# Kernel optimization log

Measured on AMD Instinct MI355X. Metric: run time of the kernel, lower is better.

Reference implementation:

```python
import jax, jax.numpy as jnp
import numpy as np

N = 50000   # nodes
F = 32      # num_node_features
EMB = 32    # embedding_size
R = 8       # num_relations
L = 5       # num_layers
E = 400000  # edges


def setup_inputs() -> dict:
    key = jax.random.key(0)
    ks = jax.random.split(key, 12)
    s = 0.1  # weight scale ~ 1/sqrt(fan_in) for stability over 5 residual layers
    return {
        "x": jax.random.normal(ks[0], (N, F), jnp.float32),
        "edge_index": jax.random.randint(ks[1], (2, E), 0, N, jnp.int32),
        "edge_type": jax.random.randint(ks[2], (E,), 0, R, jnp.int32),
        "edge_dist": jax.random.uniform(ks[3], (E,), jnp.float32),
        "fc_W": jax.random.normal(ks[4], (F, EMB), jnp.float32) * s,
        "fc_b": jnp.zeros((EMB,), jnp.float32),
        "rgcn_W": jax.random.normal(ks[5], (L, R, EMB, EMB), jnp.float32) * s,
        "rgcn_root": jax.random.normal(ks[6], (L, EMB, EMB), jnp.float32) * s,
        "rgcn_bias": jnp.zeros((L, EMB), jnp.float32),
        "mlp_W1": jax.random.normal(ks[7], (1 + R, EMB), jnp.float32) * s,
        "mlp_b1": jnp.zeros((EMB,), jnp.float32),
        "mlp_W2": jax.random.normal(ks[8], (EMB, EMB * EMB), jnp.float32) * s,
        "mlp_b2": jnp.zeros((EMB * EMB,), jnp.float32),
        "nn_root": jax.random.normal(ks[9], (L, EMB, EMB), jnp.float32) * s,
        "nn_bias": jnp.zeros((L, EMB), jnp.float32),
    }


def _forward(x, edge_index, edge_type, edge_dist, fc_W, fc_b, rgcn_W, rgcn_root,
             rgcn_bias, mlp_W1, mlp_b1, mlp_W2, mlp_b2, nn_root, nn_bias):
    n = x.shape[0]
    src, dst = edge_index[0], edge_index[1]  # source_to_target flow

    # edge_attr_c = [distance, onehot(edge_type)] : [E, 1+R]
    onehot = jax.nn.one_hot(edge_type, R, dtype=x.dtype)
    eattr = jnp.concatenate([edge_dist[:, None], onehot], axis=1)

    # Shared edge_mlp -> per-edge [EMB, EMB] weight (same for every NNConv layer)
    We = (jax.nn.relu(eattr @ mlp_W1 + mlp_b1) @ mlp_W2 + mlp_b2).reshape(-1, EMB, EMB)

    # degree for NNConv mean aggregation
    deg = jax.ops.segment_sum(jnp.ones_like(edge_dist), dst, num_segments=n)
    denom = jnp.maximum(deg, 1.0)[:, None]

    # per-relation in-degree for RGCN per-relation mean
    rel_cnt = []
    for r in range(R):
        c = jax.ops.segment_sum((edge_type == r).astype(x.dtype), dst, num_segments=n)
        rel_cnt.append(jnp.maximum(c, 1.0)[:, None])

    h = jax.nn.relu(x @ fc_W + fc_b)
    for l in range(L):
        # RGCNConv: root transform + per-relation mean of W_r x_j
        out = h @ rgcn_root[l] + rgcn_bias[l]
        for r in range(R):
            mask_r = (edge_type == r).astype(h.dtype)[:, None]
            msg = (h @ rgcn_W[l, r])[src] * mask_r  # [E, EMB]
            out = out + jax.ops.segment_sum(msg, dst, num_segments=n) / rel_cnt[r]
        h_disc = jax.nn.relu(out)

        # NNConv: x_j @ Theta(e) per edge, mean-aggregated, + root + bias
        msg = jnp.einsum('ei,eio->eo', h[src], We)  # [E, EMB]
        agg = jax.ops.segment_sum(msg, dst, num_segments=n) / denom
        h_cont = jax.nn.relu(h @ nn_root[l] + agg + nn_bias[l])

        h = h + h_disc + h_cont
    return h


def reference(x, edge_index, edge_type, edge_dist, fc_W, fc_b, rgcn_W, rgcn_root,
              rgcn_bias, mlp_W1, mlp_b1, mlp_W2, mlp_b2, nn_root, nn_bias):
    return _forward(x, edge_index, edge_type, edge_dist, fc_W, fc_b, rgcn_W,
                    rgcn_root, rgcn_bias, mlp_W1, mlp_b1, mlp_W2, mlp_b2,
                    nn_root, nn_bias)
```

## Files before the change

### kernel.cpp

```cpp
#include <hip/hip_runtime.h>

#define N_NODES 50000
#define N_EDGES 400000
#define EMB 32
#define NREL 8
#define NLAYER 5
#define NPB 16
#define NBLK (N_NODES / NPB)
#define KROWS 43
#define NCHUNK 196
#define E2CAP (N_EDGES + 8 * N_NODES)
#define FCB (N_NODES / 8)
#define FILLB ((9 * N_NODES + 255) / 256)
#define WTBFB 83

typedef __attribute__((ext_vector_type(8))) short short8;
typedef __attribute__((ext_vector_type(4))) float f32x4;
typedef __attribute__((ext_vector_type(4))) unsigned int u32x4v;

__device__ __forceinline__ unsigned short f2bf(float f) {
    unsigned u = __float_as_uint(f);
    unsigned r = u + 0x7FFF + ((u >> 16) & 1);
    return (unsigned short)(r >> 16);
}

__device__ __forceinline__ unsigned cvt_pk(float a, float b) {
    unsigned r;
    asm("v_cvt_pk_bf16_f32 %0, %1, %2" : "=v"(r) : "v"(a), "v"(b));
    return r;
}

__device__ __forceinline__ int pdeg_of(int d) {
    return (d > 0 ? d + 7 : 8) & ~7;
}


__global__ __launch_bounds__(256) void setup0_kernel(
    const float* __restrict__ x, const float* __restrict__ fcW, const float* __restrict__ fcb,
    float* __restrict__ h, unsigned short* __restrict__ hb16,
    int* __restrict__ zero9,
    unsigned* __restrict__ hb16a_pad, unsigned* __restrict__ hb16b_pad,
    const float* __restrict__ W2, const float* __restrict__ b2,
    const float* __restrict__ rgcnW, const float* __restrict__ rgcnRoot,
    const float* __restrict__ nnRoot, unsigned short* __restrict__ WB) {
    __shared__ __align__(16) float xt[8][EMB];
    const int b = blockIdx.x, tid = threadIdx.x;
    if (b < FCB) {
        int nl = tid >> 5, lane = tid & 31;
        int n0 = b * 8;
        xt[tid >> 5][tid & 31] = x[n0 * EMB + tid];
        __syncthreads();
        float acc = fcb[lane];
        #pragma unroll
        for (int i = 0; i < EMB; i++) acc += xt[nl][i] * fcW[i * EMB + lane];
        float v = fmaxf(acc, 0.0f);
        int ol = ((lane & 15) << 1) | (lane >> 4);
        h[(size_t)(n0 + nl) * EMB + ol] = v;
        float pv = __shfl_down(v, 16, 32);
        unsigned pk = cvt_pk(v, pv);
        if (lane < 16)
            *(unsigned*)&hb16[(size_t)(n0 + nl) * EMB + 2 * lane] = pk;
    } else if (b < FCB + FILLB) {
        int i = (b - FCB) * 256 + tid;
        if (i < 9 * N_NODES) zero9[i] = 0;
        if (i < EMB / 2) { hb16a_pad[i] = 0u; hb16b_pad[i] = 0u; }
    } else {
        int m = b - FCB - FILLB;
        const float* src;
        if (m < 32) src = W2 + (size_t)m * 1024;
        else if (m == 32) src = b2;
        else {
            int t = m - 33, l = t / 10, j = t % 10;
            src = (j < 8) ? rgcnW + (size_t)(l * 8 + j) * 1024
                : (j == 8) ? rgcnRoot + (size_t)l * 1024
                           : nnRoot + (size_t)l * 1024;
        }
        unsigned short* dst = WB + (size_t)m * 1024;
        #pragma unroll
        for (int c = 0; c < 4; c++) {
            int idx = c * 256 + tid;
            int o = idx >> 5, k = idx & 31;
            int i = (k >> 1) + ((k & 1) << 4);
            dst[o * 32 + k] = f2bf(src[i * 32 + o]);
        }
    }
}

__global__ __launch_bounds__(256) void hist_kernel(const int* __restrict__ ei,
                                                   const int* __restrict__ et,
                                                   int* __restrict__ relcnt) {
    int e = blockIdx.x * 256 + threadIdx.x;
    if (e < N_EDGES) {
        int d = ei[N_EDGES + e];
        atomicAdd(&relcnt[d * NREL + et[e]], 1);
    }
}

__global__ __launch_bounds__(256) void nodeprep_kernel(const int* __restrict__ relcnt,
                                                       int* __restrict__ deg,
                                                       int* __restrict__ bsum,
                                                       float* __restrict__ invdeg,
                                                       float* __restrict__ invcnt,
                                                       unsigned char* __restrict__ perm) {
    __shared__ int wsum[4];
    int tid = threadIdx.x, lane = tid & 63, wv = tid >> 6;
    int i = blockIdx.x * 256 + tid;
    int d = 0;
    if (i < N_NODES) {
        int c0 = relcnt[i * NREL + 0], c1 = relcnt[i * NREL + 1];
        int c2 = relcnt[i * NREL + 2], c3 = relcnt[i * NREL + 3];
        int c4 = relcnt[i * NREL + 4], c5 = relcnt[i * NREL + 5];
        int c6 = relcnt[i * NREL + 6], c7 = relcnt[i * NREL + 7];
        d = c0 + c1 + c2 + c3 + c4 + c5 + c6 + c7;
        deg[i] = d;
        invdeg[i] = 1.0f / (float)(d > 0 ? d : 1);
        invcnt[i * NREL + 0] = 1.0f / (float)(c0 > 0 ? c0 : 1);
        invcnt[i * NREL + 1] = 1.0f / (float)(c1 > 0 ? c1 : 1);
        invcnt[i * NREL + 2] = 1.0f / (float)(c2 > 0 ? c2 : 1);
        invcnt[i * NREL + 3] = 1.0f / (float)(c3 > 0 ? c3 : 1);
        invcnt[i * NREL + 4] = 1.0f / (float)(c4 > 0 ? c4 : 1);
        invcnt[i * NREL + 5] = 1.0f / (float)(c5 > 0 ? c5 : 1);
        invcnt[i * NREL + 6] = 1.0f / (float)(c6 > 0 ? c6 : 1);
        invcnt[i * NREL + 7] = 1.0f / (float)(c7 > 0 ? c7 : 1);
    }
    int v = (i < N_NODES) ? pdeg_of(d) : 0;
    #pragma unroll
    for (int off = 32; off > 0; off >>= 1) v += __shfl_down(v, off, 64);
    if (lane == 0) wsum[wv] = v;
    __syncthreads();
    if (tid == 0) bsum[blockIdx.x] = wsum[0] + wsum[1] + wsum[2] + wsum[3];
    if (i < NBLK) {
        int dd[NPB]; unsigned char idx[NPB];
        #pragma unroll
        for (int k = 0; k < NPB; k++) {
            int s = 0;
            #pragma unroll
            for (int r = 0; r < NREL; r++) s += relcnt[(i * NPB + k) * NREL + r];
            dd[k] = s; idx[k] = (unsigned char)k;
        }
        for (int a = 1; a < NPB; a++) {
            int dv = dd[a]; unsigned char iv = idx[a];
            int j = a - 1;
            while (j >= 0 && dd[j] < dv) { dd[j + 1] = dd[j]; idx[j + 1] = idx[j]; j--; }
            dd[j + 1] = dv; idx[j + 1] = iv;
        }
        #pragma unroll
        for (int k = 0; k < NPB; k++) perm[i * NPB + k] = idx[k];
    }
}

__global__ __launch_bounds__(256) void boff_kernel(const int* __restrict__ bsum,
                                                   int* __restrict__ boff,
                                                   int* __restrict__ row_ptr) {
    __shared__ int ws[4];
    int tid = threadIdx.x, lane = tid & 63, w = tid >> 6;
    int v = (tid < NCHUNK) ? bsum[tid] : 0;
    int incl = v;
    #pragma unroll
    for (int off = 1; off < 64; off <<= 1) {
        int t = __shfl_up(incl, off, 64);
        if (lane >= off) incl += t;
    }
    if (lane == 63) ws[w] = incl;
    __syncthreads();
    int add = 0;
    for (int j = 0; j < w; j++) add += ws[j];
    if (tid < NCHUNK) boff[tid] = add + incl - v;
    if (tid == 0) row_ptr[N_NODES] = ws[0] + ws[1] + ws[2] + ws[3];
}

__global__ __launch_bounds__(256) void rptr_kernel(const int* __restrict__ deg,
                                                   const int* __restrict__ boff,
                                                   int* __restrict__ row_ptr) {
    __shared__ int ws[4];
    int tid = threadIdx.x, lane = tid & 63, w = tid >> 6;
    int i = blockIdx.x * 256 + tid;
    int v = (i < N_NODES) ? pdeg_of(deg[i]) : 0;
    int incl = v;
    #pragma unroll
    for (int off = 1; off < 64; off <<= 1) {
        int t = __shfl_up(incl, off, 64);
        if (lane >= off) incl += t;
    }
    if (lane == 63) ws[w] = incl;
    __syncthreads();
    int add = boff[blockIdx.x];
    for (int j = 0; j < w; j++) add += ws[j];
    if (i < N_NODES) row_ptr[i] = add + incl - v;
}

__global__ __launch_bounds__(256) void scatter_kernel(const int* __restrict__ ei,
                                                      const int* __restrict__ et,
                                                      const float* __restrict__ ed,
                                                      const int* __restrict__ row_ptr,
                                                      const int* __restrict__ deg,
                                                      int* __restrict__ cursor,
                                                      int2* __restrict__ edge2,
                                                      const unsigned char* __restrict__ perm,
                                                      int4* __restrict__ wavetab) {
    int e = blockIdx.x * 256 + threadIdx.x;
    if (e < N_EDGES) {
        int d = ei[N_EDGES + e];
        int pos = row_ptr[d] + atomicAdd(&cursor[d], 1);
        edge2[pos] = make_int2(ei[e] | (et[e] << 16), __float_as_int(ed[e]));
    }
    if (e < N_NODES) {
        int base = row_ptr[e], d = deg[e], pd = pdeg_of(d);
        for (int p = base + d; p < base + pd; ++p)
            edge2[p] = make_int2(N_NODES, 0);
    }
    if (e < NBLK * 8) {
        int b = e >> 3, wv = e & 7;
        int s0 = perm[b * NPB + wv], s1 = perm[b * NPB + (NPB - 1 - wv)];
        int nA = b * NPB + s0, nB = b * NPB + s1;
        int pb0 = row_ptr[nA], pd0 = row_ptr[nA + 1] - pb0;
        int pb1 = row_ptr[nB], pd1 = row_ptr[nB + 1] - pb1;
        wavetab[e] = make_int4(s0 | (s1 << 8), pb0, pb1, pd0 | (pd1 << 16));
    }
}


__device__ __forceinline__ void gath(const unsigned short* __restrict__ hb16, int4 E, int m,
                                     unsigned& uA, unsigned& uB) {
    uA = *(const unsigned*)(hb16 + (((size_t)(E.x & 0xFFFF)) << 5) + 2 * m);
    uB = *(const unsigned*)(hb16 + (((size_t)(E.z & 0xFFFF)) << 5) + 2 * m);
}

__device__ __forceinline__ void proc_pair(int4 E, unsigned uA, unsigned uB,
                                          const float2* wrb2f, float w10_0, float w10_1,
                                          unsigned selm, int m,
                                          unsigned& A0s, unsigned& A1s, unsigned& ASs,
                                          unsigned& B0s, unsigned& B1s) {
    int ra = (E.x >> 16) & 7, rb = (E.z >> 16) & 7;
    float2 wa = wrb2f[ra * 16 + m];
    float2 wb = wrb2f[rb * 16 + m];
    float da = __int_as_float(E.y), db = __int_as_float(E.w);
    float hA0 = fmaxf(fmaf(da, w10_0, wa.x), 0.f);
    float hA1 = fmaxf(fmaf(da, w10_1, wa.y), 0.f);
    float hB0 = fmaxf(fmaf(db, w10_0, wb.x), 0.f);
    float hB1 = fmaxf(fmaf(db, w10_1, wb.y), 0.f);
    A0s = cvt_pk(hA0, hB0);
    A1s = cvt_pk(hA1, hB1);
    ASs = cvt_pk((float)((selm >> ra) & 1u), (float)((selm >> rb) & 1u));
    B0s = (uA & 0xFFFFu) | (uB << 16);
    B1s = (uA >> 16) | (uB & 0xFFFF0000u);
}

__device__ __forceinline__ void mfma6(const unsigned* fa0v, const unsigned* fa1v,
                                      const unsigned* fasv, const unsigned* fb0v,
                                      const unsigned* fb1v,
                                      f32x4& aP00, f32x4& aP01, f32x4& aP10, f32x4& aP11,
                                      f32x4& aS0, f32x4& aS1) {
    u32x4v u0 = {fa0v[0], fa0v[1], fa0v[2], fa0v[3]};
    u32x4v u1 = {fa1v[0], fa1v[1], fa1v[2], fa1v[3]};
    u32x4v us = {fasv[0], fasv[1], fasv[2], fasv[3]};
    u32x4v v0 = {fb0v[0], fb0v[1], fb0v[2], fb0v[3]};
    u32x4v v1 = {fb1v[0], fb1v[1], fb1v[2], fb1v[3]};
    short8 A0 = __builtin_bit_cast(short8, u0);
    short8 A1 = __builtin_bit_cast(short8, u1);
    short8 AS = __builtin_bit_cast(short8, us);
    short8 B0 = __builtin_bit_cast(short8, v0);
    short8 B1 = __builtin_bit_cast(short8, v1);
    aP00 = __builtin_amdgcn_mfma_f32_16x16x32_bf16(A0, B0, aP00, 0, 0, 0);
    aP01 = __builtin_amdgcn_mfma_f32_16x16x32_bf16(A0, B1, aP01, 0, 0, 0);
    aP10 = __builtin_amdgcn_mfma_f32_16x16x32_bf16(A1, B0, aP10, 0, 0, 0);
    aP11 = __builtin_amdgcn_mfma_f32_16x16x32_bf16(A1, B1, aP11, 0, 0, 0);
    aS0  = __builtin_amdgcn_mfma_f32_16x16x32_bf16(AS, B0, aS0, 0, 0, 0);
    aS1  = __builtin_amdgcn_mfma_f32_16x16x32_bf16(AS, B1, aS1, 0, 0, 0);
}

__device__ __forceinline__ void edge_pass(const unsigned short* __restrict__ hb16,
                                          const int2* __restrict__ edge2,
                                          const float2* wrb2f,
                                          int pb, int pe, int quad, int m,
                                          float w10_0, float w10_1, unsigned selm,
                                          int4 E0, unsigned u0A, unsigned u0B,
                                          f32x4& aP00, f32x4& aP01, f32x4& aP10,
                                          f32x4& aP11, f32x4& aS0, f32x4& aS1) {
    {
        unsigned fa0v[4] = {0,0,0,0}, fa1v[4] = {0,0,0,0}, fasv[4] = {0,0,0,0};
        unsigned fb0v[4] = {0,0,0,0}, fb1v[4] = {0,0,0,0};
        proc_pair(E0, u0A, u0B, wrb2f, w10_0, w10_1, selm, m,
                  fa0v[0], fa1v[0], fasv[0], fb0v[0], fb1v[0]);
        if (pb + 8 < pe) {
            int4 E = *(const int4*)&edge2[pb + 8 + quad * 2];
            unsigned uA, uB; gath(hb16, E, m, uA, uB);
            proc_pair(E, uA, uB, wrb2f, w10_0, w10_1, selm, m,
                      fa0v[1], fa1v[1], fasv[1], fb0v[1], fb1v[1]);
        }
        if (pb + 16 < pe) {
            int4 E = *(const int4*)&edge2[pb + 16 + quad * 2];
            unsigned uA, uB; gath(hb16, E, m, uA, uB);
            proc_pair(E, uA, uB, wrb2f, w10_0, w10_1, selm, m,
                      fa0v[2], fa1v[2], fasv[2], fb0v[2], fb1v[2]);
        }
        if (pb + 24 < pe) {
            int4 E = *(const int4*)&edge2[pb + 24 + quad * 2];
            unsigned uA, uB; gath(hb16, E, m, uA, uB);
            proc_pair(E, uA, uB, wrb2f, w10_0, w10_1, selm, m,
                      fa0v[3], fa1v[3], fasv[3], fb0v[3], fb1v[3]);
        }
        mfma6(fa0v, fa1v, fasv, fb0v, fb1v, aP00, aP01, aP10, aP11, aS0, aS1);
    }
    for (int c0 = pb + 32; c0 < pe; c0 += 32) {
        unsigned fa0v[4] = {0,0,0,0}, fa1v[4] = {0,0,0,0}, fasv[4] = {0,0,0,0};
        unsigned fb0v[4] = {0,0,0,0}, fb1v[4] = {0,0,0,0};
        #pragma unroll
        for (int jp = 0; jp < 4; ++jp) {
            if (c0 + jp * 8 < pe) {
                int4 E = *(const int4*)&edge2[c0 + jp * 8 + quad * 2];
                unsigned uA, uB; gath(hb16, E, m, uA, uB);
                proc_pair(E, uA, uB, wrb2f, w10_0, w10_1, selm, m,
                          fa0v[jp], fa1v[jp], fasv[jp], fb0v[jp], fb1v[jp]);
            }
        }
        mfma6(fa0v, fa1v, fasv, fb0v, fb1v, aP00, aP01, aP10, aP11, aS0, aS1);
    }
}

__device__ __forceinline__ void stage_node(unsigned short* __restrict__ P, int quad, int m,
                                           float idg, const float* __restrict__ invcnt_n,
                                           const unsigned short* __restrict__ hb16row,
                                           const f32x4& aP00, const f32x4& aP01,
                                           const f32x4& aP10, const f32x4& aP11,
                                           const f32x4& aS0, const f32x4& aS1) {
    #pragma unroll
    for (int reg = 0; reg < 4; ++reg) {
        const int row = quad * 4 + reg;
        *(unsigned*)&P[row * EMB + 2 * m]        = cvt_pk(aP00[reg] * idg, aP01[reg] * idg);
        *(unsigned*)&P[(row + 16) * EMB + 2 * m] = cvt_pk(aP10[reg] * idg, aP11[reg] * idg);
        if (row <= 8) {
            const float sc = (row == 0) ? idg : invcnt_n[row - 1];
            *(unsigned*)&P[(32 + row) * EMB + 2 * m] = cvt_pk(aS0[reg] * sc, aS1[reg] * sc);
        }
    }
    if (quad < 2) {
        unsigned hh = *(const unsigned*)(hb16row + 2 * m);
        *(unsigned*)&P[(41 + quad) * EMB + 2 * m] = hh;
    }
}

__global__ __launch_bounds__(512, 6) void layer_kernel(
    const float* __restrict__ h,
    const unsigned short* __restrict__ hb16,
    const int2* __restrict__ edge2,
    const int4* __restrict__ wavetab,
    const float* __restrict__ invdeg,
    const float* __restrict__ invcnt,
    const float* __restrict__ W1,
    const float* __restrict__ b1,
    const unsigned short* __restrict__ WBs,
    const unsigned short* __restrict__ WBl,
    const float* __restrict__ rgcnBias_l,
    const float* __restrict__ nnBias_l,
    float* __restrict__ hout,
    unsigned short* __restrict__ hb16out,
    int last)
{
    __shared__ __align__(16) unsigned short P_lds[NPB * KROWS * EMB];
    __shared__ __align__(16) float2 wrb2f[NREL * 16];

    const int tid = threadIdx.x;
    const int n0 = blockIdx.x * NPB;

    if (tid < 128) {
        int r = tid >> 4, mi = tid & 15;
        wrb2f[r * 16 + mi] = make_float2(W1[(1 + r) * EMB + mi] + b1[mi],
                                         W1[(1 + r) * EMB + mi + 16] + b1[mi + 16]);
    }

    const int l    = tid & 63;
    const int w    = tid >> 6;
    const int quad = l >> 4;
    const int m    = l & 15;
    const float w10_0 = W1[m];
    const float w10_1 = W1[m + 16];
    const unsigned selm = (m == 0) ? 0xFFu : (m <= 8 ? (1u << (m - 1)) : 0u);

    int4 wt = wavetab[blockIdx.x * 8 + w];
    const int hw0 = wt.x & 0xFF, hw1 = (wt.x >> 8) & 0xFF;
    const int pb0 = wt.y, pe0 = wt.y + (wt.w & 0xFFFF);
    const int pb1 = wt.z, pe1 = wt.z + (int)((unsigned)wt.w >> 16);
    int4 E0 = *(const int4*)&edge2[pb0 + quad * 2];
    int4 E1 = *(const int4*)&edge2[pb1 + quad * 2];
    unsigned u0A, u0B, u1A, u1B;
    gath(hb16, E0, m, u0A, u0B);
    gath(hb16, E1, m, u1A, u1B);

    __syncthreads();

    {
        f32x4 aP00 = {0,0,0,0}, aP01 = {0,0,0,0}, aP10 = {0,0,0,0}, aP11 = {0,0,0,0};
        f32x4 aS0 = {0,0,0,0}, aS1 = {0,0,0,0};
        edge_pass(hb16, edge2, wrb2f, pb0, pe0, quad, m, w10_0, w10_1, selm,
                  E0, u0A, u0B, aP00, aP01, aP10, aP11, aS0, aS1);
        const int n = n0 + hw0;
        stage_node(P_lds + (size_t)hw0 * KROWS * EMB, quad, m, invdeg[n],
                   invcnt + (size_t)n * NREL, hb16 + (size_t)n * EMB,
                   aP00, aP01, aP10, aP11, aS0, aS1);
    }
    {
        f32x4 aP00 = {0,0,0,0}, aP01 = {0,0,0,0}, aP10 = {0,0,0,0}, aP11 = {0,0,0,0};
        f32x4 aS0 = {0,0,0,0}, aS1 = {0,0,0,0};
        edge_pass(hb16, edge2, wrb2f, pb1, pe1, quad, m, w10_0, w10_1, selm,
                  E1, u1A, u1B, aP00, aP01, aP10, aP11, aS0, aS1);
        const int n = n0 + hw1;
        stage_node(P_lds + (size_t)hw1 * KROWS * EMB, quad, m, invdeg[n],
                   invcnt + (size_t)n * NREL, hb16 + (size_t)n * EMB,
                   aP00, aP01, aP10, aP11, aS0, aS1);
    }
    __syncthreads();

    const int node16 = l & 15;
    const int o0 = l & 15;

    f32x4 accN0 = {0,0,0,0}, accN1 = {0,0,0,0};
    f32x4 accR0 = {0,0,0,0}, accR1 = {0,0,0,0};

    #pragma unroll
    for (int j = 0; j < 6; j++) {
        const int rr = w + 8 * j;
        if (rr < KROWS) {
            const unsigned short* Bsrc = (rr < 33) ? (WBs + (size_t)rr * 1024)
                                                   : (WBl + (size_t)(rr - 33) * 1024);
            short8 bf0 = *(const short8*)(Bsrc + o0 * 32 + quad * 8);
            short8 bf1 = *(const short8*)(Bsrc + (o0 + 16) * 32 + quad * 8);
            short8 a = *(const short8*)&P_lds[(size_t)node16 * KROWS * EMB + rr * EMB + quad * 8];
            if (rr <= 32 || rr == 42) {
                accN0 = __builtin_amdgcn_mfma_f32_16x16x32_bf16(a, bf0, accN0, 0, 0, 0);
                accN1 = __builtin_amdgcn_mfma_f32_16x16x32_bf16(a, bf1, accN1, 0, 0, 0);
            } else {
                accR0 = __builtin_amdgcn_mfma_f32_16x16x32_bf16(a, bf0, accR0, 0, 0, 0);
                accR1 = __builtin_amdgcn_mfma_f32_16x16x32_bf16(a, bf1, accR1, 0, 0, 0);
            }
        }
    }
    __syncthreads();

    float* RedAll = (float*)&P_lds[0];
    {
        float* my = RedAll + w * 1024;
        #pragma unroll
        for (int reg = 0; reg < 4; reg++) {
            int nd = quad * 4 + reg;
            my[nd * 32 + o0]            = accN0[reg];
            my[nd * 32 + o0 + 16]       = accN1[reg];
            my[512 + nd * 32 + o0]      = accR0[reg];
            my[512 + nd * 32 + o0 + 16] = accR1[reg];
        }
    }
    __syncthreads();

    {
        const int hw2 = tid >> 5, lane = tid & 31;
        const int n2 = n0 + hw2;
        float sn = 0.0f, sr = 0.0f;
        #pragma unroll
        for (int ww = 0; ww < 8; ww++) {
            sn += RedAll[ww * 1024 + tid];
            sr += RedAll[ww * 1024 + 512 + tid];
        }
        const int il = ((lane & 15) << 1) | (lane >> 4);
        float hd = h[(size_t)n2 * EMB + il];
        float o_r = fmaxf(sr + rgcnBias_l[lane], 0.0f);
        float o_n = fmaxf(sn + nnBias_l[lane], 0.0f);
        float outv = hd + o_r + o_n;
        hout[(size_t)n2 * EMB + (last ? lane : il)] = outv;
        if (!last) {
            float pv = __shfl_down(outv, 16, 32);
            unsigned pk = cvt_pk(outv, pv);
            if (lane < 16)
                *(unsigned*)&hb16out[(size_t)n2 * EMB + 2 * lane] = pk;
        }
    }
}


extern "C" void kernel_launch(void* const* d_in, const int* in_sizes, int n_in,
                              void* d_out, int out_size, void* d_ws, size_t ws_size,
                              hipStream_t stream) {
    const float* x        = (const float*)d_in[0];
    const int*   ei       = (const int*)d_in[1];
    const int*   et       = (const int*)d_in[2];
    const float* ed       = (const float*)d_in[3];
    const float* fcW      = (const float*)d_in[4];
    const float* fcb      = (const float*)d_in[5];
    const float* rgcnW    = (const float*)d_in[6];
    const float* rgcnRoot = (const float*)d_in[7];
    const float* rgcnBias = (const float*)d_in[8];
    const float* W1       = (const float*)d_in[9];
    const float* b1       = (const float*)d_in[10];
    const float* W2       = (const float*)d_in[11];
    const float* b2       = (const float*)d_in[12];
    const float* nnRoot   = (const float*)d_in[13];
    const float* nnBias   = (const float*)d_in[14];

    float* ws = (float*)d_ws;
    float* h_a    = ws;  ws += (size_t)(N_NODES + 1) * EMB;
    float* h_b    = ws;  ws += (size_t)(N_NODES + 1) * EMB;
    unsigned short* hb16_a = (unsigned short*)ws;  ws += (size_t)(N_NODES + 1) * EMB / 2;
    unsigned short* hb16_b = (unsigned short*)ws;  ws += (size_t)(N_NODES + 1) * EMB / 2;
    float* invdeg = ws;  ws += (size_t)N_NODES;
    float* invcnt = ws;  ws += (size_t)N_NODES * NREL;
    unsigned short* WB = (unsigned short*)ws;  ws += (size_t)83 * 1024 / 2;
    int2* edge2   = (int2*)ws;     ws += (size_t)E2CAP * 2;
    int* row_ptr  = (int*)ws;      ws += (size_t)(N_NODES + 1);
    int* bsum     = (int*)ws;      ws += (size_t)NCHUNK;
    int* boff     = (int*)ws;      ws += (size_t)NCHUNK;
    int* deg      = (int*)ws;      ws += (size_t)N_NODES;
    int* relcnt   = (int*)ws;      ws += (size_t)N_NODES * NREL;
    int* cursor   = (int*)ws;      ws += (size_t)N_NODES;
    unsigned char* perm = (unsigned char*)ws;  ws += (size_t)(NBLK * NPB + 3) / 4;
    int4* wavetab = (int4*)ws;     ws += (size_t)NBLK * 8 * 4;
    (void)in_sizes; (void)n_in; (void)out_size; (void)ws_size;

    setup0_kernel<<<FCB + FILLB + WTBFB, 256, 0, stream>>>(
        x, fcW, fcb, h_a, hb16_a, relcnt,
        (unsigned*)(hb16_a + (size_t)N_NODES * EMB),
        (unsigned*)(hb16_b + (size_t)N_NODES * EMB),
        W2, b2, rgcnW, rgcnRoot, nnRoot, WB);
    hist_kernel<<<(N_EDGES + 255) / 256, 256, 0, stream>>>(ei, et, relcnt);
    nodeprep_kernel<<<NCHUNK, 256, 0, stream>>>(relcnt, deg, bsum, invdeg, invcnt, perm);
    boff_kernel<<<1, 256, 0, stream>>>(bsum, boff, row_ptr);
    rptr_kernel<<<NCHUNK, 256, 0, stream>>>(deg, boff, row_ptr);
    scatter_kernel<<<(N_EDGES + 255) / 256, 256, 0, stream>>>(ei, et, ed, row_ptr, deg,
                                                              cursor, edge2, perm, wavetab);

    const float* hin = h_a;
    const unsigned short* hbin = hb16_a;
    float* houtb = h_b;
    unsigned short* hboutb = hb16_b;
    for (int l = 0; l < NLAYER; l++) {
        int last = (l == NLAYER - 1) ? 1 : 0;
        float* dst = last ? (float*)d_out : houtb;
        layer_kernel<<<NBLK, 512, 0, stream>>>(
            hin, hbin, edge2, wavetab, invdeg, invcnt, W1, b1,
            WB, WB + (size_t)(33 + l * 10) * 1024,
            rgcnBias + (size_t)l * EMB,
            nnBias + (size_t)l * EMB,
            dst, hboutb, last);
        float* old_in = (float*)hin;
        unsigned short* old_hb = (unsigned short*)hbin;
        hin = dst; hbin = hboutb;
        houtb = old_in; hboutb = old_hb;
    }
}
```

Baseline: 368.6 us.

## Use one wave per node with 1024-thread blocks, dropping degree-sorted wave pairing

The layer kernel now launches 16 waves per block, so each wave handles a single node's edges directly through row_ptr. This replaces the earlier scheme of pairing heavy and light nodes per wave from a degree-sorted permutation and wavetab, and the perm and wavetab setup code is removed. The weight-row GEMM loop is split across 16 waves, and the cross-wave reduction gains a second accumulate stage. The LDS table stride is padded from 16 to 17 to avoid bank conflicts. In exchange, load balance within a wave is lost for skewed degrees, and larger blocks may reduce occupancy flexibility.

```diff
diff --git a/kernel.cpp b/kernel.cpp
--- a/kernel.cpp
+++ b/kernel.cpp
@@ -100,8 +100,7 @@
                                                        int* __restrict__ deg,
                                                        int* __restrict__ bsum,
                                                        float* __restrict__ invdeg,
-                                                       float* __restrict__ invcnt,
-                                                       unsigned char* __restrict__ perm) {
+                                                       float* __restrict__ invcnt) {
     __shared__ int wsum[4];
     int tid = threadIdx.x, lane = tid & 63, wv = tid >> 6;
     int i = blockIdx.x * 256 + tid;
@@ -129,24 +128,6 @@
     if (lane == 0) wsum[wv] = v;
     __syncthreads();
     if (tid == 0) bsum[blockIdx.x] = wsum[0] + wsum[1] + wsum[2] + wsum[3];
-    if (i < NBLK) {
-        int dd[NPB]; unsigned char idx[NPB];
-        #pragma unroll
-        for (int k = 0; k < NPB; k++) {
-            int s = 0;
-            #pragma unroll
-            for (int r = 0; r < NREL; r++) s += relcnt[(i * NPB + k) * NREL + r];
-            dd[k] = s; idx[k] = (unsigned char)k;
-        }
-        for (int a = 1; a < NPB; a++) {
-            int dv = dd[a]; unsigned char iv = idx[a];
-            int j = a - 1;
-            while (j >= 0 && dd[j] < dv) { dd[j + 1] = dd[j]; idx[j + 1] = idx[j]; j--; }
-            dd[j + 1] = dv; idx[j + 1] = iv;
-        }
-        #pragma unroll
-        for (int k = 0; k < NPB; k++) perm[i * NPB + k] = idx[k];
-    }
 }
 
 __global__ __launch_bounds__(256) void boff_kernel(const int* __restrict__ bsum,
@@ -195,9 +176,7 @@
                                                       const int* __restrict__ row_ptr,
                                                       const int* __restrict__ deg,
                                                       int* __restrict__ cursor,
-                                                      int2* __restrict__ edge2,
-                                                      const unsigned char* __restrict__ perm,
-                                                      int4* __restrict__ wavetab) {
+                                                      int2* __restrict__ edge2) {
     int e = blockIdx.x * 256 + threadIdx.x;
     if (e < N_EDGES) {
         int d = ei[N_EDGES + e];
@@ -208,14 +187,6 @@
         int base = row_ptr[e], d = deg[e], pd = pdeg_of(d);
         for (int p = base + d; p < base + pd; ++p)
             edge2[p] = make_int2(N_NODES, 0);
-    }
-    if (e < NBLK * 8) {
-        int b = e >> 3, wv = e & 7;
-        int s0 = perm[b * NPB + wv], s1 = perm[b * NPB + (NPB - 1 - wv)];
-        int nA = b * NPB + s0, nB = b * NPB + s1;
-        int pb0 = row_ptr[nA], pd0 = row_ptr[nA + 1] - pb0;
-        int pb1 = row_ptr[nB], pd1 = row_ptr[nB + 1] - pb1;
-        wavetab[e] = make_int4(s0 | (s1 << 8), pb0, pb1, pd0 | (pd1 << 16));
     }
 }
 
@@ -232,8 +203,8 @@
                                           unsigned& A0s, unsigned& A1s, unsigned& ASs,
                                           unsigned& B0s, unsigned& B1s) {
     int ra = (E.x >> 16) & 7, rb = (E.z >> 16) & 7;
-    float2 wa = wrb2f[ra * 16 + m];
-    float2 wb = wrb2f[rb * 16 + m];
+    float2 wa = wrb2f[ra * 17 + m];
+    float2 wb = wrb2f[rb * 17 + m];
     float da = __int_as_float(E.y), db = __int_as_float(E.w);
     float hA0 = fmaxf(fmaf(da, w10_0, wa.x), 0.f);
     float hA1 = fmaxf(fmaf(da, w10_1, wa.y), 0.f);
@@ -340,11 +311,11 @@
     }
 }
 
-__global__ __launch_bounds__(512, 6) void layer_kernel(
+__global__ __launch_bounds__(1024, 4) void layer_kernel(
     const float* __restrict__ h,
     const unsigned short* __restrict__ hb16,
     const int2* __restrict__ edge2,
-    const int4* __restrict__ wavetab,
+    const int* __restrict__ row_ptr,
     const float* __restrict__ invdeg,
     const float* __restrict__ invcnt,
     const float* __restrict__ W1,
@@ -358,14 +329,14 @@
     int last)
 {
     __shared__ __align__(16) unsigned short P_lds[NPB * KROWS * EMB];
-    __shared__ __align__(16) float2 wrb2f[NREL * 16];
+    __shared__ __align__(16) float2 wrb2f[NREL * 17];
 
     const int tid = threadIdx.x;
     const int n0 = blockIdx.x * NPB;
 
     if (tid < 128) {
         int r = tid >> 4, mi = tid & 15;
-        wrb2f[r * 16 + mi] = make_float2(W1[(1 + r) * EMB + mi] + b1[mi],
+        wrb2f[r * 17 + mi] = make_float2(W1[(1 + r) * EMB + mi] + b1[mi],
                                          W1[(1 + r) * EMB + mi + 16] + b1[mi + 16]);
     }
 
@@ -377,38 +348,23 @@
     const float w10_1 = W1[m + 16];
     const unsigned selm = (m == 0) ? 0xFFu : (m <= 8 ? (1u << (m - 1)) : 0u);
 
-    int4 wt = wavetab[blockIdx.x * 8 + w];
-    const int hw0 = wt.x & 0xFF, hw1 = (wt.x >> 8) & 0xFF;
-    const int pb0 = wt.y, pe0 = wt.y + (wt.w & 0xFFFF);
-    const int pb1 = wt.z, pe1 = wt.z + (int)((unsigned)wt.w >> 16);
-    int4 E0 = *(const int4*)&edge2[pb0 + quad * 2];
-    int4 E1 = *(const int4*)&edge2[pb1 + quad * 2];
-    unsigned u0A, u0B, u1A, u1B;
+    const int n  = n0 + w;
+    const int pb = row_ptr[n], pe = row_ptr[n + 1];
+    int4 E0 = *(const int4*)&edge2[pb + quad * 2];
+    unsigned u0A, u0B;
     gath(hb16, E0, m, u0A, u0B);
-    gath(hb16, E1, m, u1A, u1B);
 
     __syncthreads();
 
     {
         f32x4 aP00 = {0,0,0,0}, aP01 = {0,0,0,0}, aP10 = {0,0,0,0}, aP11 = {0,0,0,0};
         f32x4 aS0 = {0,0,0,0}, aS1 = {0,0,0,0};
-        edge_pass(hb16, edge2, wrb2f, pb0, pe0, quad, m, w10_0, w10_1, selm,
+        edge_pass(hb16, edge2, wrb2f, pb, pe, quad, m, w10_0, w10_1, selm,
                   E0, u0A, u0B, aP00, aP01, aP10, aP11, aS0, aS1);
-        const int n = n0 + hw0;
-        stage_node(P_lds + (size_t)hw0 * KROWS * EMB, quad, m, invdeg[n],
+        stage_node(P_lds + (size_t)w * KROWS * EMB, quad, m, invdeg[n],
                    invcnt + (size_t)n * NREL, hb16 + (size_t)n * EMB,
                    aP00, aP01, aP10, aP11, aS0, aS1);
     }
-    {
-        f32x4 aP00 = {0,0,0,0}, aP01 = {0,0,0,0}, aP10 = {0,0,0,0}, aP11 = {0,0,0,0};
-        f32x4 aS0 = {0,0,0,0}, aS1 = {0,0,0,0};
-        edge_pass(hb16, edge2, wrb2f, pb1, pe1, quad, m, w10_0, w10_1, selm,
-                  E1, u1A, u1B, aP00, aP01, aP10, aP11, aS0, aS1);
-        const int n = n0 + hw1;
-        stage_node(P_lds + (size_t)hw1 * KROWS * EMB, quad, m, invdeg[n],
-                   invcnt + (size_t)n * NREL, hb16 + (size_t)n * EMB,
-                   aP00, aP01, aP10, aP11, aS0, aS1);
-    }
     __syncthreads();
 
     const int node16 = l & 15;
@@ -418,8 +374,8 @@
     f32x4 accR0 = {0,0,0,0}, accR1 = {0,0,0,0};
 
     #pragma unroll
-    for (int j = 0; j < 6; j++) {
-        const int rr = w + 8 * j;
+    for (int j = 0; j < 3; j++) {
+        const int rr = w + 16 * j;
         if (rr < KROWS) {
             const unsigned short* Bsrc = (rr < 33) ? (WBs + (size_t)rr * 1024)
                                                    : (WBl + (size_t)(rr - 33) * 1024);
@@ -438,7 +394,7 @@
     __syncthreads();
 
     float* RedAll = (float*)&P_lds[0];
-    {
+    if (w < 8) {
         float* my = RedAll + w * 1024;
         #pragma unroll
         for (int reg = 0; reg < 4; reg++) {
@@ -450,8 +406,20 @@
         }
     }
     __syncthreads();
-
-    {
+    if (w >= 8) {
+        float* my = RedAll + (w - 8) * 1024;
+        #pragma unroll
+        for (int reg = 0; reg < 4; reg++) {
+            int nd = quad * 4 + reg;
+            my[nd * 32 + o0]            += accN0[reg];
+            my[nd * 32 + o0 + 16]       += accN1[reg];
+            my[512 + nd * 32 + o0]      += accR0[reg];
+            my[512 + nd * 32 + o0 + 16] += accR1[reg];
+        }
+    }
+    __syncthreads();
+
+    if (tid < 512) {
         const int hw2 = tid >> 5, lane = tid & 31;
         const int n2 = n0 + hw2;
         float sn = 0.0f, sr = 0.0f;
@@ -510,8 +478,6 @@
     int* deg      = (int*)ws;      ws += (size_t)N_NODES;
     int* relcnt   = (int*)ws;      ws += (size_t)N_NODES * NREL;
     int* cursor   = (int*)ws;      ws += (size_t)N_NODES;
-    unsigned char* perm = (unsigned char*)ws;  ws += (size_t)(NBLK * NPB + 3) / 4;
-    int4* wavetab = (int4*)ws;     ws += (size_t)NBLK * 8 * 4;
     (void)in_sizes; (void)n_in; (void)out_size; (void)ws_size;
 
     setup0_kernel<<<FCB + FILLB + WTBFB, 256, 0, stream>>>(
@@ -520,11 +486,11 @@
         (unsigned*)(hb16_b + (size_t)N_NODES * EMB),
         W2, b2, rgcnW, rgcnRoot, nnRoot, WB);
     hist_kernel<<<(N_EDGES + 255) / 256, 256, 0, stream>>>(ei, et, relcnt);
-    nodeprep_kernel<<<NCHUNK, 256, 0, stream>>>(relcnt, deg, bsum, invdeg, invcnt, perm);
+    nodeprep_kernel<<<NCHUNK, 256, 0, stream>>>(relcnt, deg, bsum, invdeg, invcnt);
     boff_kernel<<<1, 256, 0, stream>>>(bsum, boff, row_ptr);
     rptr_kernel<<<NCHUNK, 256, 0, stream>>>(deg, boff, row_ptr);
     scatter_kernel<<<(N_EDGES + 255) / 256, 256, 0, stream>>>(ei, et, ed, row_ptr, deg,
-                                                              cursor, edge2, perm, wavetab);
+                                                              cursor, edge2);
 
     const float* hin = h_a;
     const unsigned short* hbin = hb16_a;
@@ -533,8 +499,8 @@
     for (int l = 0; l < NLAYER; l++) {
         int last = (l == NLAYER - 1) ? 1 : 0;
         float* dst = last ? (float*)d_out : houtb;
-        layer_kernel<<<NBLK, 512, 0, stream>>>(
-            hin, hbin, edge2, wavetab, invdeg, invcnt, W1, b1,
+        layer_kernel<<<NBLK, 1024, 0, stream>>>(
+            hin, hbin, edge2, row_ptr, invdeg, invcnt, W1, b1,
             WB, WB + (size_t)(33 + l * 10) * 1024,
             rgcnBias + (size_t)l * EMB,
             nnBias + (size_t)l * EMB,
```

Result: slower. 484.9 us (+31.5%).
